# Kernel optimization log

Hardware: AMD Instinct MI355X
Metric: run time of the kernel (lower is better)

## Reference

```python
import jax, jax.numpy as jnp
import numpy as np
from jax.scipy.special import logsumexp


def setup_inputs() -> dict:
    key = jax.random.key(0)
    k1, k2 = jax.random.split(key)
    B, T, V = 128, 128, 32000
    inputs = jax.random.normal(k1, (B, T), dtype=jnp.float32)
    # LDA init stddev = sqrt((1/beta)*(1 - 1/V)) with beta = 1/V
    stddev = ((1.0 / (1.0 / V)) * (1.0 - 1.0 / V)) ** 0.5
    w = jax.random.normal(k2, (T, V), dtype=jnp.float32) * jnp.float32(stddev)
    return {"inputs": inputs, "w": w}


def reference(inputs, w):
    # inputs: (B, T) unnormalized log topic weights; w: (T, V) unnormalized log word dists
    # inference path: no dropout (training=None)
    log_theta = inputs - logsumexp(inputs, axis=1, keepdims=True)   # (B, T)
    log_phi = w - logsumexp(w, axis=1, keepdims=True)               # (T, V)
    # log-domain matmul: z[b, v] = logsumexp_t(log_theta[b, t] + log_phi[t, v])
    z = logsumexp(log_theta[:, :, None] + log_phi[None, :, :], axis=1)  # (B, V)
    return z
```

## Files before the change

### kernel.cpp

```cpp
#include <hip/hip_runtime.h>
#include <math.h>


constexpr int B = 128;
constexpr int T = 128;
constexpr int V = 32000;
constexpr int VC = 64;
constexpr int KPARTS = 4;
constexpr int PART = V / KPARTS;

constexpr int WS_EA = 0;
constexpr int WS_PM = 8192;
constexpr int WS_PS = WS_PM + T * KPARTS;
constexpr int WS_GT = WS_PS + T * KPARTS;

typedef __attribute__((ext_vector_type(8))) short bf16x8;
typedef __attribute__((ext_vector_type(4))) float f32x4;
typedef __attribute__((ext_vector_type(4))) unsigned u32x4;

__device__ inline unsigned short f2bf(float f) {
    union { float f; unsigned u; } x; x.f = f;
    unsigned u = x.u + 0x7fff + ((x.u >> 16) & 1);
    return (unsigned short)(u >> 16);
}

__device__ inline int swz_word(int row, int tp) {
    return (((tp >> 2) ^ (row & 15)) << 2) | (tp & 3);
}

__global__ __launch_bounds__(256) void k_stage1(const float* __restrict__ inp,
                                                const float* __restrict__ w,
                                                float* __restrict__ pm,
                                                float* __restrict__ ps,
                                                float* __restrict__ gt_out,
                                                unsigned* __restrict__ Ea) {
    __shared__ float sh[B * (T + 1)];
    __shared__ float gts[T];
    const int tid = threadIdx.x;

    if (blockIdx.x != 0) {
        const int bid = blockIdx.x - 1;
        const int t = bid >> 2;
        const int part = bid & 3;
        const float4* row = (const float4*)(w + (size_t)t * V + (size_t)part * PART);

        float m = -INFINITY, s = 0.f;
        for (int i = tid; i < PART / 4; i += 256) {
            float4 x4 = row[i];
            float xs[4] = {x4.x, x4.y, x4.z, x4.w};
            #pragma unroll
            for (int j = 0; j < 4; ++j) {
                float x = xs[j];
                float mn = fmaxf(m, x);
                s = s * __expf(m - mn) + __expf(x - mn);
                m = mn;
            }
        }
        float* sm = sh;
        float* ss = sh + 256;
        sm[tid] = m; ss[tid] = s;
        __syncthreads();
        for (int off = 128; off > 0; off >>= 1) {
            if (tid < off) {
                float m1 = sm[tid],       s1 = ss[tid];
                float m2 = sm[tid + off], s2 = ss[tid + off];
                float M = fmaxf(m1, m2);
                sm[tid] = M;
                ss[tid] = s1 * __expf(m1 - M) + s2 * __expf(m2 - M);
            }
            __syncthreads();
        }
        if (tid == 0) { pm[bid] = sm[0]; ps[bid] = ss[0]; }
        return;
    }

    #pragma unroll
    for (int k = 0; k < 16; ++k) {
        int i4 = tid + k * 256;
        float4 x = ((const float4*)inp)[i4];
        int r = i4 >> 5, c = (i4 & 31) * 4;
        float* dst = &sh[r * 129 + c];
        dst[0] = x.x; dst[1] = x.y; dst[2] = x.z; dst[3] = x.w;
    }
    __syncthreads();

    if (tid < B) {
        const int b = tid;
        const float* row = &sh[b * 129];
        float m = -INFINITY;
        for (int t = 0; t < T; ++t) m = fmaxf(m, row[t]);
        float s = 0.f;
        for (int t = 0; t < T; ++t) s += __expf(row[t] - m);
        sh[b * 129 + 128] = m + logf(s);
    }
    __syncthreads();

    if (tid < T) {
        const int t = tid;
        float g = -INFINITY;
        for (int b = 0; b < B; ++b) g = fmaxf(g, sh[b * 129 + t] - sh[b * 129 + 128]);
        gts[t] = g;
        gt_out[t] = g;
    }
    __syncthreads();

    if (tid < B) {
        const int b = tid;
        const float li = sh[b * 129 + 128];
        unsigned pk[64];
        #pragma unroll
        for (int tp = 0; tp < 64; ++tp) {
            float e0 = __expf(sh[b * 129 + 2 * tp]     - li - gts[2 * tp]);
            float e1 = __expf(sh[b * 129 + 2 * tp + 1] - li - gts[2 * tp + 1]);
            pk[tp] = (unsigned)f2bf(e0) | ((unsigned)f2bf(e1) << 16);
        }
        unsigned* row = (unsigned*)&sh[b * 129];
        #pragma unroll
        for (int tp = 0; tp < 64; ++tp) row[swz_word(b, tp)] = pk[tp];
    }
    __syncthreads();

    #pragma unroll
    for (int k = 0; k < 32; ++k) {
        int d = tid + k * 256;
        int b = d >> 6, wsw = d & 63;
        Ea[d] = ((unsigned*)&sh[b * 129])[wsw];
    }
}

__global__ __launch_bounds__(256) void k_main(const float* __restrict__ w,
                                              const float* __restrict__ pm,
                                              const float* __restrict__ ps,
                                              const float* __restrict__ gt,
                                              const unsigned* __restrict__ Ea_g,
                                              float* __restrict__ out) {
    __shared__ unsigned EaL[B * 64];
    __shared__ unsigned EwL[VC * 64];
    __shared__ float cs[T];
    __shared__ float mu[VC];
    __shared__ float pmH[4][VC];

    const int tid = threadIdx.x;
    const int vbase = blockIdx.x * VC;

    if (tid < T) {
        const int t = tid;
        float M = pm[t * KPARTS];
        #pragma unroll
        for (int p = 1; p < KPARTS; ++p) M = fmaxf(M, pm[t * KPARTS + p]);
        float S = 0.f;
        #pragma unroll
        for (int p = 0; p < KPARTS; ++p) S += ps[t * KPARTS + p] * __expf(pm[t * KPARTS + p] - M);
        cs[t] = gt[t] - (M + logf(S));
    }

    {
        const float4* src = (const float4*)Ea_g;
        float4* dst = (float4*)EaL;
        #pragma unroll
        for (int k = 0; k < 8; ++k) dst[tid + k * 256] = src[tid + k * 256];
    }
    __syncthreads();

    const int v = tid & 63, q = tid >> 6;
    {
        const float* col = w + vbase + v;
        float m = -INFINITY;
        #pragma unroll 8
        for (int t = q * 32; t < q * 32 + 32; ++t)
            m = fmaxf(m, col[(size_t)t * V] + cs[t]);
        pmH[q][v] = m;
    }
    __syncthreads();
    if (tid < VC)
        mu[tid] = fmaxf(fmaxf(pmH[0][tid], pmH[1][tid]), fmaxf(pmH[2][tid], pmH[3][tid]));
    __syncthreads();

    {
        const float m_ = mu[v];
        #pragma unroll
        for (int gi = 0; gi < 4; ++gi) {
            const int g2 = q * 4 + gi;
            unsigned pk[4];
            #pragma unroll
            for (int i = 0; i < 4; ++i) {
                int tp = g2 * 4 + i;
                float w0 = w[(size_t)(2 * tp) * V + vbase + v];
                float w1 = w[(size_t)(2 * tp + 1) * V + vbase + v];
                float e0 = __expf(w0 + cs[2 * tp] - m_);
                float e1 = __expf(w1 + cs[2 * tp + 1] - m_);
                pk[i] = (unsigned)f2bf(e0) | ((unsigned)f2bf(e1) << 16);
            }
            u32x4* dst = (u32x4*)&EwL[v * 64 + ((g2 ^ (v & 15)) << 2)];
            *dst = (u32x4){pk[0], pk[1], pk[2], pk[3]};
        }
    }
    __syncthreads();

    const int lane = tid & 63;
    const int wave = tid >> 6;
    const int wb = (wave >> 1) * 64;
    const int wv = (wave & 1) * 32;
    const int r = lane & 15;
    const int g = lane >> 4;

    f32x4 acc[4][2];
    #pragma unroll
    for (int m = 0; m < 4; ++m)
        #pragma unroll
        for (int n = 0; n < 2; ++n) acc[m][n] = (f32x4){0.f, 0.f, 0.f, 0.f};

    #pragma unroll
    for (int kk = 0; kk < 4; ++kk) {
        const int grp = kk * 4 + g;
        bf16x8 af[4], bfr[2];
        #pragma unroll
        for (int m = 0; m < 4; ++m) {
            int bb = wb + m * 16 + r;
            af[m] = *(const bf16x8*)((const char*)EaL + bb * 256 + ((grp ^ (bb & 15)) << 4));
        }
        #pragma unroll
        for (int n = 0; n < 2; ++n) {
            int vv = wv + n * 16 + r;
            bfr[n] = *(const bf16x8*)((const char*)EwL + vv * 256 + ((grp ^ (vv & 15)) << 4));
        }
        #pragma unroll
        for (int m = 0; m < 4; ++m)
            #pragma unroll
            for (int n = 0; n < 2; ++n)
                acc[m][n] = __builtin_amdgcn_mfma_f32_16x16x32_bf16(af[m], bfr[n], acc[m][n], 0, 0, 0);
    }

    #pragma unroll
    for (int m = 0; m < 4; ++m) {
        int bb = wb + m * 16 + g * 4;
        #pragma unroll
        for (int n = 0; n < 2; ++n) {
            float muv = mu[wv + n * 16 + r];
            size_t col = (size_t)(vbase + wv + n * 16 + r);
            #pragma unroll
            for (int j = 0; j < 4; ++j)
                out[(size_t)(bb + j) * V + col] = muv + __logf(acc[m][n][j]);
        }
    }
}

extern "C" void kernel_launch(void* const* d_in, const int* in_sizes, int n_in,
                              void* d_out, int out_size, void* d_ws, size_t ws_size,
                              hipStream_t stream) {
    const float* inp = (const float*)d_in[0];
    const float* w   = (const float*)d_in[1];
    float* out = (float*)d_out;
    unsigned* ws = (unsigned*)d_ws;

    unsigned* Ea = ws + WS_EA;
    float* pm = (float*)(ws + WS_PM);
    float* ps = (float*)(ws + WS_PS);
    float* gt = (float*)(ws + WS_GT);

    k_stage1<<<dim3(T * KPARTS + 1), dim3(256), 0, stream>>>(inp, w, pm, ps, gt, Ea);
    k_main<<<dim3(V / VC), dim3(256), 0, stream>>>(w, pm, ps, gt, Ea, out);
}
```

Baseline: 34.64 us.

## Load w tile once into registers in main kernel; two-pass row logsumexp

The main kernel now loads its 128x64 slice of w into registers once, as float4 vectors at the start, before the cs computation and Ea copy. It reuses those registers for both the column max and the exp/bf16 packing, where the old code read each w column from global memory twice with scalar loads. Stage 1 replaces the online per-element max/rescale logsumexp with a max pass followed by a sum-of-exp pass, which drops the per-element rescaling exp. In exchange the w row is read twice from memory or L2, and the register tile costs 32 extra VGPRs per thread.

```diff
diff --git a/kernel.cpp b/kernel.cpp
--- a/kernel.cpp
+++ b/kernel.cpp
@@ -44,33 +44,33 @@
         const int part = bid & 3;
         const float4* row = (const float4*)(w + (size_t)t * V + (size_t)part * PART);
 
-        float m = -INFINITY, s = 0.f;
+        float m = -INFINITY;
         for (int i = tid; i < PART / 4; i += 256) {
             float4 x4 = row[i];
-            float xs[4] = {x4.x, x4.y, x4.z, x4.w};
-            #pragma unroll
-            for (int j = 0; j < 4; ++j) {
-                float x = xs[j];
-                float mn = fmaxf(m, x);
-                s = s * __expf(m - mn) + __expf(x - mn);
-                m = mn;
-            }
+            m = fmaxf(fmaxf(m, fmaxf(x4.x, x4.y)), fmaxf(x4.z, x4.w));
         }
         float* sm = sh;
-        float* ss = sh + 256;
-        sm[tid] = m; ss[tid] = s;
+        sm[tid] = m;
         __syncthreads();
         for (int off = 128; off > 0; off >>= 1) {
-            if (tid < off) {
-                float m1 = sm[tid],       s1 = ss[tid];
-                float m2 = sm[tid + off], s2 = ss[tid + off];
-                float M = fmaxf(m1, m2);
-                sm[tid] = M;
-                ss[tid] = s1 * __expf(m1 - M) + s2 * __expf(m2 - M);
-            }
+            if (tid < off) sm[tid] = fmaxf(sm[tid], sm[tid + off]);
             __syncthreads();
         }
-        if (tid == 0) { pm[bid] = sm[0]; ps[bid] = ss[0]; }
+        const float M = sm[0];
+
+        float s = 0.f;
+        for (int i = tid; i < PART / 4; i += 256) {
+            float4 x4 = row[i];
+            s += __expf(x4.x - M) + __expf(x4.y - M) + __expf(x4.z - M) + __expf(x4.w - M);
+        }
+        float* ss = sh + 256;
+        ss[tid] = s;
+        __syncthreads();
+        for (int off = 128; off > 0; off >>= 1) {
+            if (tid < off) ss[tid] += ss[tid + off];
+            __syncthreads();
+        }
+        if (tid == 0) { pm[bid] = M; ps[bid] = ss[0]; }
         return;
     }
 
@@ -138,10 +138,20 @@
     __shared__ unsigned EwL[VC * 64];
     __shared__ float cs[T];
     __shared__ float mu[VC];
-    __shared__ float pmH[4][VC];
+    __shared__ float pmT[VC][17];
 
     const int tid = threadIdx.x;
     const int vbase = blockIdx.x * VC;
+    const int v4 = tid & 15;
+    const int tq = tid >> 4;
+
+    f32x4 wr[8];
+    {
+        const float* wp = w + (size_t)(tq * 8) * V + vbase + v4 * 4;
+        #pragma unroll
+        for (int i = 0; i < 8; ++i)
+            wr[i] = *(const f32x4*)(wp + (size_t)i * V);
+    }
 
     if (tid < T) {
         const int t = tid;
@@ -162,37 +172,43 @@
     }
     __syncthreads();
 
-    const int v = tid & 63, q = tid >> 6;
-    {
-        const float* col = w + vbase + v;
-        float m = -INFINITY;
-        #pragma unroll 8
-        for (int t = q * 32; t < q * 32 + 32; ++t)
-            m = fmaxf(m, col[(size_t)t * V] + cs[t]);
-        pmH[q][v] = m;
-    }
-    __syncthreads();
-    if (tid < VC)
-        mu[tid] = fmaxf(fmaxf(pmH[0][tid], pmH[1][tid]), fmaxf(pmH[2][tid], pmH[3][tid]));
-    __syncthreads();
-
-    {
-        const float m_ = mu[v];
-        #pragma unroll
-        for (int gi = 0; gi < 4; ++gi) {
-            const int g2 = q * 4 + gi;
+    {
+        float p0 = -INFINITY, p1 = -INFINITY, p2 = -INFINITY, p3 = -INFINITY;
+        #pragma unroll
+        for (int i = 0; i < 8; ++i) {
+            const float cc = cs[tq * 8 + i];
+            p0 = fmaxf(p0, wr[i][0] + cc);
+            p1 = fmaxf(p1, wr[i][1] + cc);
+            p2 = fmaxf(p2, wr[i][2] + cc);
+            p3 = fmaxf(p3, wr[i][3] + cc);
+        }
+        pmT[v4 * 4 + 0][tq] = p0;
+        pmT[v4 * 4 + 1][tq] = p1;
+        pmT[v4 * 4 + 2][tq] = p2;
+        pmT[v4 * 4 + 3][tq] = p3;
+    }
+    __syncthreads();
+    if (tid < VC) {
+        float m = pmT[tid][0];
+        #pragma unroll
+        for (int r = 1; r < 16; ++r) m = fmaxf(m, pmT[tid][r]);
+        mu[tid] = m;
+    }
+    __syncthreads();
+
+    {
+        #pragma unroll
+        for (int c = 0; c < 4; ++c) {
+            const int v = v4 * 4 + c;
+            const float m_ = mu[v];
             unsigned pk[4];
             #pragma unroll
-            for (int i = 0; i < 4; ++i) {
-                int tp = g2 * 4 + i;
-                float w0 = w[(size_t)(2 * tp) * V + vbase + v];
-                float w1 = w[(size_t)(2 * tp + 1) * V + vbase + v];
-                float e0 = __expf(w0 + cs[2 * tp] - m_);
-                float e1 = __expf(w1 + cs[2 * tp + 1] - m_);
-                pk[i] = (unsigned)f2bf(e0) | ((unsigned)f2bf(e1) << 16);
+            for (int p2 = 0; p2 < 4; ++p2) {
+                float e0 = __expf(wr[2 * p2][c]     + cs[tq * 8 + 2 * p2]     - m_);
+                float e1 = __expf(wr[2 * p2 + 1][c] + cs[tq * 8 + 2 * p2 + 1] - m_);
+                pk[p2] = (unsigned)f2bf(e0) | ((unsigned)f2bf(e1) << 16);
             }
-            u32x4* dst = (u32x4*)&EwL[v * 64 + ((g2 ^ (v & 15)) << 2)];
-            *dst = (u32x4){pk[0], pk[1], pk[2], pk[3]};
+            *(u32x4*)&EwL[v * 64 + ((tq ^ (v & 15)) << 2)] = (u32x4){pk[0], pk[1], pk[2], pk[3]};
         }
     }
     __syncthreads();
```

After: 30.08 us. 13.2% less time.
